# Kernel tuning notes

Hardware: AMD Instinct MI355X
Metric: run time of the kernel (lower is better)

Reference implementation:

```python
import jax, jax.numpy as jnp
import numpy as np

B, N1, N2, D = 8, 2048, 2048, 512

def setup_inputs() -> dict:
    key = jax.random.key(0)
    k1, k2, k3, k4 = jax.random.split(key, 4)
    input1 = jax.random.normal(k1, (B, N1, D), dtype=jnp.float32)
    input2 = jax.random.normal(k2, (B, N2, D), dtype=jnp.float32)
    # nn.Linear(D, D): weight [D, D] (out, in), bias [D]
    W_w = jax.random.normal(k3, (D, D), dtype=jnp.float32) * (1.0 / np.sqrt(D))
    W_b = jax.random.normal(k4, (D,), dtype=jnp.float32) * 0.01
    return {"input1": input1, "input2": input2, "W_w": W_w, "W_b": W_b}

def reference(input1, input2, W_w, W_b):
    # q = W(input1): [B, N1, D]
    q = jnp.einsum('bnd,od->bno', input1, W_w) + W_b
    # unscaled scores softmax over last dim (keys N2)
    attn = jax.nn.softmax(jnp.einsum('bnd,bmd->bnm', q, input2), axis=-1)  # [B, N1, N2]
    output1 = jnp.einsum('bnm,bmd->bnd', attn, input2)   # [B, N1, D]
    output2 = jnp.einsum('bnm,bnd->bmd', attn, input1)   # attn^T @ input1 -> [B, N2, D]
    return (output1, output2)
```

## Files before the change

kernel.cpp:

```cpp
#include <hip/hip_runtime.h>


typedef _Float16 f16x8 __attribute__((ext_vector_type(8)));
typedef _Float16 f16x4 __attribute__((ext_vector_type(4)));
typedef float floatx4 __attribute__((ext_vector_type(4)));
typedef __attribute__((address_space(1))) const void* gptr_t;
typedef __attribute__((address_space(3))) void* lptr_t;

union F8 { f16x8 v; _Float16 h[8]; unsigned short u[8]; unsigned w[4]; };
union F4 { f16x4 v; _Float16 h[4]; unsigned u2[2]; };

__device__ __forceinline__ void gld16(const void* g, void* l) {
    __builtin_amdgcn_global_load_lds((gptr_t)g, (lptr_t)l, 16, 0, 0);
}
__device__ __forceinline__ floatx4 mfma16(f16x8 a, f16x8 b, floatx4 c) {
    return __builtin_amdgcn_mfma_f32_16x16x32_f16(a, b, c, 0, 0, 0);
}

template <int ROWS>
__device__ __forceinline__ void stage64(const _Float16* g, int ldg,
                                        _Float16* lds, int tid) {
#pragma unroll
    for (int c = 0; c < (ROWS * 8) / 256; ++c) {
        const int q = c * 256 + tid;
        const int row = q >> 3;
        const int oct = (q & 7) ^ (row & 7);
        gld16(g + (size_t)row * ldg + oct * 8, lds + q * 8);
    }
}
__device__ __forceinline__ f16x8 ldfrag64(const _Float16* lds, int row, int j) {
    return *(const f16x8*)&lds[row * 64 + ((j ^ (row & 7)) << 3)];
}

template <int ROWS>
__device__ __forceinline__ void stage128(const _Float16* g, int ldg,
                                         _Float16* lds, int tid) {
#pragma unroll
    for (int c = 0; c < (ROWS * 16) / 256; ++c) {
        const int q = c * 256 + tid;
        const int row = q >> 4;
        const int oct = (q & 15) ^ (row & 15);
        gld16(g + (size_t)row * ldg + oct * 8, lds + q * 8);
    }
}
__device__ __forceinline__ f16x8 ldfrag128(const _Float16* lds, int row, int j) {
    return *(const f16x8*)&lds[row * 128 + ((j ^ (row & 15)) << 3)];
}

#define TS 66
__global__ __launch_bounds__(256) void k_prep2(
    const float* __restrict__ in1, const float* __restrict__ in2,
    _Float16* __restrict__ x16, _Float16* __restrict__ xt,
    _Float16* __restrict__ k16, _Float16* __restrict__ vt)
{
    __shared__ __align__(16) _Float16 T[64 * TS];
    const int z = blockIdx.z;
    const int b = z & 7;
    const float* src = (z < 8 ? in1 : in2);
    _Float16* rowo = (z < 8 ? x16 : k16);
    _Float16* colo = (z < 8 ? xt : vt);
    const int d0 = blockIdx.x * 64, n0 = blockIdx.y * 64;
    const float* Sp = src + (size_t)b * 2048 * 512;
    _Float16* Rp = rowo + (size_t)b * 2048 * 512;
    _Float16* Cp = colo + (size_t)b * 512 * 2048;
    const int t = threadIdx.x;

#pragma unroll
    for (int c = 0; c < 4; c++) {
        const int q = c * 256 + t, r = q >> 4, c4 = q & 15;
        const float4 g = *(const float4*)(Sp + (size_t)(n0 + r) * 512 + d0 + c4 * 4);
        F4 w;
        w.h[0] = (_Float16)g.x; w.h[1] = (_Float16)g.y;
        w.h[2] = (_Float16)g.z; w.h[3] = (_Float16)g.w;
        *(f16x4*)(Rp + (size_t)(n0 + r) * 512 + d0 + c4 * 4) = w.v;
        *(unsigned*)&T[r * TS + c4 * 4]     = w.u2[0];
        *(unsigned*)&T[r * TS + c4 * 4 + 2] = w.u2[1];
    }
    __syncthreads();
    const int c8 = t & 7, drp = (t >> 3) * 2;
    F8 w0, w1;
#pragma unroll
    for (int i = 0; i < 8; i++) {
        const unsigned g = *(const unsigned*)&T[(c8 * 8 + i) * TS + drp];
        w0.u[i] = (unsigned short)(g & 0xffffu);
        w1.u[i] = (unsigned short)(g >> 16);
    }
    *(f16x8*)(Cp + (size_t)(d0 + drp) * 2048 + n0 + c8 * 8) = w0.v;
    *(f16x8*)(Cp + (size_t)(d0 + drp + 1) * 2048 + n0 + c8 * 8) = w1.v;
}

__global__ __launch_bounds__(256) void k_cvt(const float* __restrict__ src,
                                             _Float16* __restrict__ dst)
{
    const size_t i = ((size_t)blockIdx.x * 256 + threadIdx.x) * 8;
    float4 a = *(const float4*)(src + i);
    float4 b = *(const float4*)(src + i + 4);
    F8 w;
    w.h[0] = (_Float16)a.x; w.h[1] = (_Float16)a.y;
    w.h[2] = (_Float16)a.z; w.h[3] = (_Float16)a.w;
    w.h[4] = (_Float16)b.x; w.h[5] = (_Float16)b.y;
    w.h[6] = (_Float16)b.z; w.h[7] = (_Float16)b.w;
    *(f16x8*)(dst + i) = w.v;
}

__global__ __launch_bounds__(256, 4) void k_qgemm16(
    const _Float16* __restrict__ A, const _Float16* __restrict__ W,
    const float* __restrict__ bias, _Float16* __restrict__ q)
{
    __shared__ __align__(16) _Float16 As[128 * 64], Bs[128 * 64];
    const int tid = threadIdx.x;
    const int lane = tid & 63, wave = tid >> 6;
    const int wM = (wave >> 1) * 64, wN = (wave & 1) * 64;
    const int lrow = lane & 15, kq = lane >> 4;
    const int bi = blockIdx.x;
    const int r0 = (bi >> 2) * 128, c0 = (bi & 3) * 128;

    floatx4 acc[4][4];
#pragma unroll
    for (int i = 0; i < 4; i++)
#pragma unroll
        for (int j = 0; j < 4; j++) acc[i][j] = (floatx4){0.f, 0.f, 0.f, 0.f};

    for (int k0 = 0; k0 < 512; k0 += 64) {
        stage64<128>(A + (size_t)r0 * 512 + k0, 512, As, tid);
        stage64<128>(W + (size_t)c0 * 512 + k0, 512, Bs, tid);
        __syncthreads();
#pragma unroll
        for (int ks = 0; ks < 2; ks++) {
            f16x8 a[4], b[4];
#pragma unroll
            for (int i = 0; i < 4; i++) {
                a[i] = ldfrag64(As, wM + i * 16 + lrow, ks * 4 + kq);
                b[i] = ldfrag64(Bs, wN + i * 16 + lrow, ks * 4 + kq);
            }
#pragma unroll
            for (int mi = 0; mi < 4; mi++)
#pragma unroll
                for (int ni = 0; ni < 4; ni++)
                    acc[mi][ni] = mfma16(a[mi], b[ni], acc[mi][ni]);
        }
        __syncthreads();
    }
#pragma unroll
    for (int ni = 0; ni < 4; ni++) {
        const int col = c0 + wN + ni * 16 + lrow;
        const float bv = bias[col];
#pragma unroll
        for (int mi = 0; mi < 4; mi++) {
            const int row = r0 + wM + mi * 16 + kq * 4;
#pragma unroll
            for (int r = 0; r < 4; r++)
                q[(size_t)(row + r) * 512 + col] = (_Float16)(acc[mi][ni][r] + bv);
        }
    }
}

__global__ __launch_bounds__(256, 4) void k_scores16(
    const _Float16* __restrict__ q, const _Float16* __restrict__ k,
    _Float16* __restrict__ S)
{
    __shared__ __align__(16) _Float16 As[128 * 64], Bs[128 * 64];
    const int tid = threadIdx.x;
    const int lane = tid & 63, wave = tid >> 6;
    const int wM = (wave >> 1) * 64, wN = (wave & 1) * 64;
    const int lrow = lane & 15, kq = lane >> 4;
    const int bi = blockIdx.x;
    const int bz = bi & 7, t = bi >> 3;
    const int c0 = (t & 15) * 128, r0 = (t >> 4) * 128;
    const _Float16* qp = q + (size_t)bz * 2048 * 512;
    const _Float16* kp = k + (size_t)bz * 2048 * 512;
    _Float16* Sp = S + (size_t)bz * 2048 * 2048;

    floatx4 acc[4][4];
#pragma unroll
    for (int i = 0; i < 4; i++)
#pragma unroll
        for (int j = 0; j < 4; j++) acc[i][j] = (floatx4){0.f, 0.f, 0.f, 0.f};

    for (int k0 = 0; k0 < 512; k0 += 64) {
        stage64<128>(qp + (size_t)r0 * 512 + k0, 512, As, tid);
        stage64<128>(kp + (size_t)c0 * 512 + k0, 512, Bs, tid);
        __syncthreads();
#pragma unroll
        for (int ks = 0; ks < 2; ks++) {
            f16x8 a[4], b[4];
#pragma unroll
            for (int i = 0; i < 4; i++) {
                a[i] = ldfrag64(As, wM + i * 16 + lrow, ks * 4 + kq);
                b[i] = ldfrag64(Bs, wN + i * 16 + lrow, ks * 4 + kq);
            }
#pragma unroll
            for (int mi = 0; mi < 4; mi++)
#pragma unroll
                for (int ni = 0; ni < 4; ni++)
                    acc[mi][ni] = mfma16(a[mi], b[ni], acc[mi][ni]);
        }
        __syncthreads();
    }
#pragma unroll
    for (int mi = 0; mi < 4; mi++)
#pragma unroll
        for (int ni = 0; ni < 4; ni++) {
            const int row = r0 + wM + mi * 16 + kq * 4;
            const int col = c0 + wN + ni * 16 + lrow;
            _Float16* dst = Sp + (size_t)row * 2048 + col;
#pragma unroll
            for (int r = 0; r < 4; r++) dst[(size_t)r * 2048] = (_Float16)acc[mi][ni][r];
        }
}

__global__ __launch_bounds__(256) void k_softmax(const _Float16* __restrict__ S,
                                                 _Float16* __restrict__ P)
{
    const int wave = threadIdx.x >> 6, lane = threadIdx.x & 63;
    const int row = blockIdx.x * 4 + wave;
    const _Float16* s = S + (size_t)row * 2048;
    _Float16* p = P + (size_t)row * 2048;

    F8 raw[4];
    float v[32];
#pragma unroll
    for (int c = 0; c < 4; c++) {
        raw[c].v = *(const f16x8*)(s + c * 512 + lane * 8);
#pragma unroll
        for (int i = 0; i < 8; i++) v[c * 8 + i] = (float)raw[c].h[i];
    }
    float m = v[0];
#pragma unroll
    for (int i = 1; i < 32; i++) m = fmaxf(m, v[i]);
#pragma unroll
    for (int off = 32; off >= 1; off >>= 1) m = fmaxf(m, __shfl_xor(m, off));

    float sum = 0.f;
#pragma unroll
    for (int i = 0; i < 32; i++) { v[i] = __expf(v[i] - m); sum += v[i]; }
#pragma unroll
    for (int off = 32; off >= 1; off >>= 1) sum += __shfl_xor(sum, off);
    const float inv = 1.0f / sum;

#pragma unroll
    for (int c = 0; c < 4; c++) {
        F8 w;
#pragma unroll
        for (int i = 0; i < 8; i++) w.h[i] = (_Float16)(v[c * 8 + i] * inv);
        *(f16x8*)(p + c * 512 + lane * 8) = w.v;
    }
}

__global__ __launch_bounds__(256, 3) void k_out1(
    const _Float16* __restrict__ P, const _Float16* __restrict__ Vt,
    float* __restrict__ O1)
{
    __shared__ __align__(16) _Float16 As[2][64 * 64], Bs[2][128 * 64];
    const int tid = threadIdx.x;
    const int lane = tid & 63, wave = tid >> 6;
    const int wM = (wave >> 1) * 32, wN = (wave & 1) * 64;
    const int lrow = lane & 15, kq = lane >> 4;
    const int bi = blockIdx.x;
    const int bz = bi & 7, t = bi >> 3;
    const int c0 = (t & 3) * 128, r0 = (t >> 2) * 64;
    const _Float16* Pp = P + (size_t)bz * 2048 * 2048;
    const _Float16* Bp = Vt + (size_t)bz * 512 * 2048;
    float* Op = O1 + (size_t)bz * 2048 * 512;

    floatx4 acc[2][4];
#pragma unroll
    for (int i = 0; i < 2; i++)
#pragma unroll
        for (int j = 0; j < 4; j++) acc[i][j] = (floatx4){0.f, 0.f, 0.f, 0.f};

    stage64<64>(Pp + (size_t)r0 * 2048, 2048, As[0], tid);
    stage64<128>(Bp + (size_t)c0 * 2048, 2048, Bs[0], tid);
    int cur = 0;
    for (int k0 = 0; k0 < 2048; k0 += 64) {
        if (k0 < 2048 - 64) {
            stage64<64>(Pp + (size_t)r0 * 2048 + k0 + 64, 2048, As[cur ^ 1], tid);
            stage64<128>(Bp + (size_t)c0 * 2048 + k0 + 64, 2048, Bs[cur ^ 1], tid);
            asm volatile("s_waitcnt vmcnt(6)" ::: "memory");
        } else {
            asm volatile("s_waitcnt vmcnt(0)" ::: "memory");
        }
        __builtin_amdgcn_s_barrier();
        const _Float16* Ac = As[cur];
        const _Float16* Bc = Bs[cur];
#pragma unroll
        for (int ks = 0; ks < 2; ks++) {
            f16x8 a[2], b[4];
#pragma unroll
            for (int i = 0; i < 2; i++)
                a[i] = ldfrag64(Ac, wM + i * 16 + lrow, ks * 4 + kq);
#pragma unroll
            for (int i = 0; i < 4; i++)
                b[i] = ldfrag64(Bc, wN + i * 16 + lrow, ks * 4 + kq);
#pragma unroll
            for (int mi = 0; mi < 2; mi++)
#pragma unroll
                for (int ni = 0; ni < 4; ni++)
                    acc[mi][ni] = mfma16(a[mi], b[ni], acc[mi][ni]);
        }
        __builtin_amdgcn_s_barrier();
        cur ^= 1;
    }
#pragma unroll
    for (int mi = 0; mi < 2; mi++)
#pragma unroll
        for (int ni = 0; ni < 4; ni++) {
            const int row = r0 + wM + mi * 16 + kq * 4;
            const int col = c0 + wN + ni * 16 + lrow;
            float* dst = Op + (size_t)row * 512 + col;
#pragma unroll
            for (int r = 0; r < 4; r++) dst[(size_t)r * 512] = acc[mi][ni][r];
        }
}

__device__ __forceinline__ void loadtr(const _Float16* Pp, int r0, int mPair,
                                       int kOct0, int k0, unsigned (&u)[16]) {
#pragma unroll
    for (int kh = 0; kh < 2; kh++)
#pragma unroll
        for (int j = 0; j < 8; j++)
            u[kh * 8 + j] = *(const unsigned*)(
                Pp + (size_t)(k0 + (kOct0 + kh * 8) * 8 + j) * 2048 + r0 + mPair);
}

__global__ __launch_bounds__(256, 2) void k_out2(
    const _Float16* __restrict__ P, const _Float16* __restrict__ Xt,
    float* __restrict__ O2)
{
    __shared__ __align__(16) _Float16 As[64 * 128];
    __shared__ __align__(16) _Float16 Bs[2][128 * 128];
    const int tid = threadIdx.x;
    const int lane = tid & 63, wave = tid >> 6;
    const int wM = (wave >> 1) * 32, wN = (wave & 1) * 64;
    const int lrow = lane & 15, kq = lane >> 4;
    const int bi = blockIdx.x;
    const int bz = bi & 7, t = bi >> 3;
    const int c0 = (t & 3) * 128, r0 = (t >> 2) * 64;
    const _Float16* Pp = P + (size_t)bz * 2048 * 2048;
    const _Float16* Bp = Xt + (size_t)bz * 512 * 2048;
    float* Op = O2 + (size_t)bz * 2048 * 512;

    const int mPair = (tid & 31) * 2;
    const int kOct0 = tid >> 5;

    floatx4 acc[2][4];
#pragma unroll
    for (int i = 0; i < 2; i++)
#pragma unroll
        for (int j = 0; j < 4; j++) acc[i][j] = (floatx4){0.f, 0.f, 0.f, 0.f};

    unsigned u[16];
    loadtr(Pp, r0, mPair, kOct0, 0, u);
    stage128<128>(Bp + (size_t)c0 * 2048, 2048, Bs[0], tid);
    int cur = 0;
    for (int k0 = 0; k0 < 2048; k0 += 128) {
#pragma unroll
        for (int kh = 0; kh < 2; kh++) {
            const int kOct = kOct0 + kh * 8;
            F8 w0, w1;
#pragma unroll
            for (int j = 0; j < 8; j++) {
                const unsigned g = u[kh * 8 + j];
                w0.u[j] = (unsigned short)(g & 0xffffu);
                w1.u[j] = (unsigned short)(g >> 16);
            }
            *(f16x8*)&As[mPair * 128 + ((kOct ^ (mPair & 15)) << 3)] = w0.v;
            *(f16x8*)&As[(mPair + 1) * 128 + ((kOct ^ ((mPair + 1) & 15)) << 3)] = w1.v;
        }
        if (k0 < 2048 - 128) {
            loadtr(Pp, r0, mPair, kOct0, k0 + 128, u);
            stage128<128>(Bp + (size_t)c0 * 2048 + k0 + 128, 2048,
                          Bs[cur ^ 1], tid);
            asm volatile("s_waitcnt vmcnt(20) lgkmcnt(0)" ::: "memory");
        } else {
            asm volatile("s_waitcnt vmcnt(0) lgkmcnt(0)" ::: "memory");
        }
        __builtin_amdgcn_s_barrier();
        const _Float16* Bc = Bs[cur];
#pragma unroll
        for (int ks = 0; ks < 4; ks++) {
            f16x8 a[2], b[4];
#pragma unroll
            for (int i = 0; i < 2; i++)
                a[i] = ldfrag128(As, wM + i * 16 + lrow, ks * 4 + kq);
#pragma unroll
            for (int i = 0; i < 4; i++)
                b[i] = ldfrag128(Bc, wN + i * 16 + lrow, ks * 4 + kq);
#pragma unroll
            for (int mi = 0; mi < 2; mi++)
#pragma unroll
                for (int ni = 0; ni < 4; ni++)
                    acc[mi][ni] = mfma16(a[mi], b[ni], acc[mi][ni]);
        }
        __builtin_amdgcn_s_barrier();
        cur ^= 1;
    }
#pragma unroll
    for (int mi = 0; mi < 2; mi++)
#pragma unroll
        for (int ni = 0; ni < 4; ni++) {
            const int row = r0 + wM + mi * 16 + kq * 4;
            const int col = c0 + wN + ni * 16 + lrow;
            float* dst = Op + (size_t)row * 512 + col;
#pragma unroll
            for (int r = 0; r < 4; r++) dst[(size_t)r * 512] = acc[mi][ni][r];
        }
}

extern "C" void kernel_launch(void* const* d_in, const int* in_sizes, int n_in,
                              void* d_out, int out_size, void* d_ws, size_t ws_size,
                              hipStream_t stream)
{
    (void)in_sizes; (void)n_in; (void)out_size; (void)ws_size;
    const float* in1 = (const float*)d_in[0];
    const float* in2 = (const float*)d_in[1];
    const float* Ww  = (const float*)d_in[2];
    const float* Wb  = (const float*)d_in[3];
    float* out = (float*)d_out;

    char* ws = (char*)d_ws;
    _Float16* S   = (_Float16*)ws;
    _Float16* P   = (_Float16*)(ws + 67108864ull);
    _Float16* q16 = (_Float16*)(ws + 134217728ull);
    _Float16* x16 = (_Float16*)(ws + 150994944ull);
    _Float16* k16 = (_Float16*)(ws + 167772160ull);
    _Float16* vt  = (_Float16*)(ws + 184549376ull);
    _Float16* xt  = (_Float16*)(ws + 201326592ull);
    _Float16* w16 = (_Float16*)(ws + 218103808ull);

    k_prep2<<<dim3(8, 32, 16), 256, 0, stream>>>(in1, in2, x16, xt, k16, vt);
    k_cvt <<<128, 256, 0, stream>>>(Ww, w16);
    k_qgemm16<<<512, 256, 0, stream>>>(x16, w16, Wb, q16);
    k_scores16<<<2048, 256, 0, stream>>>(q16, k16, S);
    k_softmax<<<4096, 256, 0, stream>>>(S, P);
    k_out2<<<1024, 256, 0, stream>>>(P, xt, out + 8388608);
    k_out1<<<1024, 256, 0, stream>>>(P, vt, out);
}
```

Baseline: 295.6 us.

## Merge out1 and out2 GEMMs into one launch with larger 128x128 tiles

```diff
diff --git a/kernel.cpp b/kernel.cpp
--- a/kernel.cpp
+++ b/kernel.cpp
@@ -31,20 +31,8 @@
 __device__ __forceinline__ f16x8 ldfrag64(const _Float16* lds, int row, int j) {
     return *(const f16x8*)&lds[row * 64 + ((j ^ (row & 7)) << 3)];
 }
-
-template <int ROWS>
-__device__ __forceinline__ void stage128(const _Float16* g, int ldg,
-                                         _Float16* lds, int tid) {
-#pragma unroll
-    for (int c = 0; c < (ROWS * 16) / 256; ++c) {
-        const int q = c * 256 + tid;
-        const int row = q >> 4;
-        const int oct = (q & 15) ^ (row & 15);
-        gld16(g + (size_t)row * ldg + oct * 8, lds + q * 8);
-    }
-}
-__device__ __forceinline__ f16x8 ldfrag128(const _Float16* lds, int row, int j) {
-    return *(const f16x8*)&lds[row * 128 + ((j ^ (row & 15)) << 3)];
+__device__ __forceinline__ f16x8 ldfragA(const _Float16* lds, int row, int j) {
+    return *(const f16x8*)&lds[row * 64 + ((j ^ ((row >> 1) & 7)) << 3)];
 }
 
 #define TS 66
@@ -247,156 +235,126 @@
     }
 }
 
-__global__ __launch_bounds__(256, 3) void k_out1(
+__device__ __forceinline__ void loadtr16(const _Float16* Pp, int r0, int mPair,
+                                         int kBase, int k0, unsigned (&u)[16]) {
+#pragma unroll
+    for (int j = 0; j < 16; j++)
+        u[j] = *(const unsigned*)(
+            Pp + (size_t)(k0 + kBase + j) * 2048 + r0 + mPair);
+}
+
+__global__ __launch_bounds__(256, 2) void k_out12(
     const _Float16* __restrict__ P, const _Float16* __restrict__ Vt,
-    float* __restrict__ O1)
-{
-    __shared__ __align__(16) _Float16 As[2][64 * 64], Bs[2][128 * 64];
+    const _Float16* __restrict__ Xt, float* __restrict__ O1,
+    float* __restrict__ O2)
+{
+    __shared__ __align__(16) _Float16 lds[32768];
     const int tid = threadIdx.x;
     const int lane = tid & 63, wave = tid >> 6;
-    const int wM = (wave >> 1) * 32, wN = (wave & 1) * 64;
+    const int wM = (wave >> 1) * 64, wN = (wave & 1) * 64;
     const int lrow = lane & 15, kq = lane >> 4;
-    const int bi = blockIdx.x;
+    const bool isO2 = blockIdx.x & 1;
+    const int bi = blockIdx.x >> 1;
     const int bz = bi & 7, t = bi >> 3;
-    const int c0 = (t & 3) * 128, r0 = (t >> 2) * 64;
+    const int c0 = (t & 3) * 128, r0 = (t >> 2) * 128;
     const _Float16* Pp = P + (size_t)bz * 2048 * 2048;
-    const _Float16* Bp = Vt + (size_t)bz * 512 * 2048;
-    float* Op = O1 + (size_t)bz * 2048 * 512;
-
-    floatx4 acc[2][4];
-#pragma unroll
-    for (int i = 0; i < 2; i++)
+    const _Float16* Bp = (isO2 ? Xt : Vt) + (size_t)bz * 512 * 2048;
+    float* Op = (isO2 ? O2 : O1) + (size_t)bz * 2048 * 512;
+
+    floatx4 acc[4][4];
+#pragma unroll
+    for (int i = 0; i < 4; i++)
 #pragma unroll
         for (int j = 0; j < 4; j++) acc[i][j] = (floatx4){0.f, 0.f, 0.f, 0.f};
 
-    stage64<64>(Pp + (size_t)r0 * 2048, 2048, As[0], tid);
-    stage64<128>(Bp + (size_t)c0 * 2048, 2048, Bs[0], tid);
-    int cur = 0;
-    for (int k0 = 0; k0 < 2048; k0 += 64) {
-        if (k0 < 2048 - 64) {
-            stage64<64>(Pp + (size_t)r0 * 2048 + k0 + 64, 2048, As[cur ^ 1], tid);
-            stage64<128>(Bp + (size_t)c0 * 2048 + k0 + 64, 2048, Bs[cur ^ 1], tid);
-            asm volatile("s_waitcnt vmcnt(6)" ::: "memory");
-        } else {
-            asm volatile("s_waitcnt vmcnt(0)" ::: "memory");
-        }
-        __builtin_amdgcn_s_barrier();
-        const _Float16* Ac = As[cur];
-        const _Float16* Bc = Bs[cur];
-#pragma unroll
-        for (int ks = 0; ks < 2; ks++) {
-            f16x8 a[2], b[4];
-#pragma unroll
-            for (int i = 0; i < 2; i++)
-                a[i] = ldfrag64(Ac, wM + i * 16 + lrow, ks * 4 + kq);
-#pragma unroll
-            for (int i = 0; i < 4; i++)
-                b[i] = ldfrag64(Bc, wN + i * 16 + lrow, ks * 4 + kq);
-#pragma unroll
-            for (int mi = 0; mi < 2; mi++)
-#pragma unroll
-                for (int ni = 0; ni < 4; ni++)
-                    acc[mi][ni] = mfma16(a[mi], b[ni], acc[mi][ni]);
-        }
-        __builtin_amdgcn_s_barrier();
-        cur ^= 1;
-    }
-#pragma unroll
-    for (int mi = 0; mi < 2; mi++)
-#pragma unroll
-        for (int ni = 0; ni < 4; ni++) {
-            const int row = r0 + wM + mi * 16 + kq * 4;
-            const int col = c0 + wN + ni * 16 + lrow;
-            float* dst = Op + (size_t)row * 512 + col;
-#pragma unroll
-            for (int r = 0; r < 4; r++) dst[(size_t)r * 512] = acc[mi][ni][r];
-        }
-}
-
-__device__ __forceinline__ void loadtr(const _Float16* Pp, int r0, int mPair,
-                                       int kOct0, int k0, unsigned (&u)[16]) {
-#pragma unroll
-    for (int kh = 0; kh < 2; kh++)
-#pragma unroll
-        for (int j = 0; j < 8; j++)
-            u[kh * 8 + j] = *(const unsigned*)(
-                Pp + (size_t)(k0 + (kOct0 + kh * 8) * 8 + j) * 2048 + r0 + mPair);
-}
-
-__global__ __launch_bounds__(256, 2) void k_out2(
-    const _Float16* __restrict__ P, const _Float16* __restrict__ Xt,
-    float* __restrict__ O2)
-{
-    __shared__ __align__(16) _Float16 As[64 * 128];
-    __shared__ __align__(16) _Float16 Bs[2][128 * 128];
-    const int tid = threadIdx.x;
-    const int lane = tid & 63, wave = tid >> 6;
-    const int wM = (wave >> 1) * 32, wN = (wave & 1) * 64;
-    const int lrow = lane & 15, kq = lane >> 4;
-    const int bi = blockIdx.x;
-    const int bz = bi & 7, t = bi >> 3;
-    const int c0 = (t & 3) * 128, r0 = (t >> 2) * 64;
-    const _Float16* Pp = P + (size_t)bz * 2048 * 2048;
-    const _Float16* Bp = Xt + (size_t)bz * 512 * 2048;
-    float* Op = O2 + (size_t)bz * 2048 * 512;
-
-    const int mPair = (tid & 31) * 2;
-    const int kOct0 = tid >> 5;
-
-    floatx4 acc[2][4];
-#pragma unroll
-    for (int i = 0; i < 2; i++)
-#pragma unroll
-        for (int j = 0; j < 4; j++) acc[i][j] = (floatx4){0.f, 0.f, 0.f, 0.f};
-
-    unsigned u[16];
-    loadtr(Pp, r0, mPair, kOct0, 0, u);
-    stage128<128>(Bp + (size_t)c0 * 2048, 2048, Bs[0], tid);
-    int cur = 0;
-    for (int k0 = 0; k0 < 2048; k0 += 128) {
-#pragma unroll
-        for (int kh = 0; kh < 2; kh++) {
-            const int kOct = kOct0 + kh * 8;
-            F8 w0, w1;
-#pragma unroll
-            for (int j = 0; j < 8; j++) {
-                const unsigned g = u[kh * 8 + j];
-                w0.u[j] = (unsigned short)(g & 0xffffu);
-                w1.u[j] = (unsigned short)(g >> 16);
-            }
-            *(f16x8*)&As[mPair * 128 + ((kOct ^ (mPair & 15)) << 3)] = w0.v;
-            *(f16x8*)&As[(mPair + 1) * 128 + ((kOct ^ ((mPair + 1) & 15)) << 3)] = w1.v;
-        }
-        if (k0 < 2048 - 128) {
-            loadtr(Pp, r0, mPair, kOct0, k0 + 128, u);
-            stage128<128>(Bp + (size_t)c0 * 2048 + k0 + 128, 2048,
-                          Bs[cur ^ 1], tid);
-            asm volatile("s_waitcnt vmcnt(20) lgkmcnt(0)" ::: "memory");
-        } else {
-            asm volatile("s_waitcnt vmcnt(0) lgkmcnt(0)" ::: "memory");
-        }
-        __builtin_amdgcn_s_barrier();
-        const _Float16* Bc = Bs[cur];
-#pragma unroll
-        for (int ks = 0; ks < 4; ks++) {
-            f16x8 a[2], b[4];
-#pragma unroll
-            for (int i = 0; i < 2; i++)
-                a[i] = ldfrag128(As, wM + i * 16 + lrow, ks * 4 + kq);
-#pragma unroll
-            for (int i = 0; i < 4; i++)
-                b[i] = ldfrag128(Bc, wN + i * 16 + lrow, ks * 4 + kq);
-#pragma unroll
-            for (int mi = 0; mi < 2; mi++)
-#pragma unroll
-                for (int ni = 0; ni < 4; ni++)
-                    acc[mi][ni] = mfma16(a[mi], b[ni], acc[mi][ni]);
-        }
-        __builtin_amdgcn_s_barrier();
-        cur ^= 1;
-    }
-#pragma unroll
-    for (int mi = 0; mi < 2; mi++)
+    if (!isO2) {
+        stage64<128>(Pp + (size_t)r0 * 2048, 2048, lds, tid);
+        stage64<128>(Bp + (size_t)c0 * 2048, 2048, lds + 16384, tid);
+        int cur = 0;
+        for (int k0 = 0; k0 < 2048; k0 += 64) {
+            if (k0 < 2048 - 64) {
+                stage64<128>(Pp + (size_t)r0 * 2048 + k0 + 64, 2048,
+                             lds + (cur ^ 1) * 8192, tid);
+                stage64<128>(Bp + (size_t)c0 * 2048 + k0 + 64, 2048,
+                             lds + 16384 + (cur ^ 1) * 8192, tid);
+                asm volatile("s_waitcnt vmcnt(8)" ::: "memory");
+            } else {
+                asm volatile("s_waitcnt vmcnt(0)" ::: "memory");
+            }
+            __builtin_amdgcn_s_barrier();
+            const _Float16* Ac = lds + cur * 8192;
+            const _Float16* Bc = lds + 16384 + cur * 8192;
+#pragma unroll
+            for (int ks = 0; ks < 2; ks++) {
+                f16x8 a[4], b[4];
+#pragma unroll
+                for (int i = 0; i < 4; i++) {
+                    a[i] = ldfrag64(Ac, wM + i * 16 + lrow, ks * 4 + kq);
+                    b[i] = ldfrag64(Bc, wN + i * 16 + lrow, ks * 4 + kq);
+                }
+#pragma unroll
+                for (int mi = 0; mi < 4; mi++)
+#pragma unroll
+                    for (int ni = 0; ni < 4; ni++)
+                        acc[mi][ni] = mfma16(a[mi], b[ni], acc[mi][ni]);
+            }
+            __builtin_amdgcn_s_barrier();
+            cur ^= 1;
+        }
+    } else {
+        _Float16* As_ = lds;
+        const int mPair = (tid & 63) * 2;
+        const int kBase = (tid >> 6) * 16;
+
+        unsigned u[16];
+        loadtr16(Pp, r0, mPair, kBase, 0, u);
+        stage64<128>(Bp + (size_t)c0 * 2048, 2048, lds + 8192, tid);
+        int cur = 0;
+        for (int k0 = 0; k0 < 2048; k0 += 64) {
+            const int sw = (mPair >> 1) & 7;
+#pragma unroll
+            for (int half = 0; half < 2; half++) {
+                const int oct = (kBase >> 3) + half;
+                F8 w0, w1;
+#pragma unroll
+                for (int j = 0; j < 8; j++) {
+                    const unsigned g = u[half * 8 + j];
+                    w0.u[j] = (unsigned short)(g & 0xffffu);
+                    w1.u[j] = (unsigned short)(g >> 16);
+                }
+                *(f16x8*)&As_[mPair * 64 + ((oct ^ sw) << 3)] = w0.v;
+                *(f16x8*)&As_[(mPair + 1) * 64 + ((oct ^ sw) << 3)] = w1.v;
+            }
+            if (k0 < 2048 - 64) {
+                loadtr16(Pp, r0, mPair, kBase, k0 + 64, u);
+                stage64<128>(Bp + (size_t)c0 * 2048 + k0 + 64, 2048,
+                             lds + 8192 + (cur ^ 1) * 8192, tid);
+                asm volatile("s_waitcnt vmcnt(20) lgkmcnt(0)" ::: "memory");
+            } else {
+                asm volatile("s_waitcnt vmcnt(0) lgkmcnt(0)" ::: "memory");
+            }
+            __builtin_amdgcn_s_barrier();
+            const _Float16* Bc = lds + 8192 + cur * 8192;
+#pragma unroll
+            for (int ks = 0; ks < 2; ks++) {
+                f16x8 a[4], b[4];
+#pragma unroll
+                for (int i = 0; i < 4; i++) {
+                    a[i] = ldfragA(As_, wM + i * 16 + lrow, ks * 4 + kq);
+                    b[i] = ldfrag64(Bc, wN + i * 16 + lrow, ks * 4 + kq);
+                }
+#pragma unroll
+                for (int mi = 0; mi < 4; mi++)
+#pragma unroll
+                    for (int ni = 0; ni < 4; ni++)
+                        acc[mi][ni] = mfma16(a[mi], b[ni], acc[mi][ni]);
+            }
+            __builtin_amdgcn_s_barrier();
+            cur ^= 1;
+        }
+    }
+#pragma unroll
+    for (int mi = 0; mi < 4; mi++)
 #pragma unroll
         for (int ni = 0; ni < 4; ni++) {
             const int row = r0 + wM + mi * 16 + kq * 4;
@@ -433,6 +391,5 @@
     k_qgemm16<<<512, 256, 0, stream>>>(x16, w16, Wb, q16);
     k_scores16<<<2048, 256, 0, stream>>>(q16, k16, S);
     k_softmax<<<4096, 256, 0, stream>>>(S, P);
-    k_out2<<<1024, 256, 0, stream>>>(P, xt, out + 8388608);
-    k_out1<<<1024, 256, 0, stream>>>(P, vt, out);
-}
+    k_out12<<<1024, 256, 0, stream>>>(P, vt, xt, out, out + 8388608);
+}
```

Measured after the change: 272.9 us. 7.7% less time.
